# Kernel optimization log

Measured on AMD Instinct MI355X. Metric: run time of the kernel, lower is better.

The kernel has to match this reference:

```python
import jax, jax.numpy as jnp
import numpy as np

NEG_SLOPE = 0.2  # PyG GATConv default negative_slope


def gat_layer(x, W, a_src, a_dst, bias, src, dst, num_nodes):
    # x: [N, Fin], W: [Fin, H*C], a_src/a_dst: [H, C], bias: [C]
    H, C = a_src.shape
    h = (x @ W).reshape(num_nodes, H, C)                      # [N, H, C]
    alpha_src = jnp.einsum('nhc,hc->nh', h, a_src)            # [N, H]
    alpha_dst = jnp.einsum('nhc,hc->nh', h, a_dst)            # [N, H]
    e = jax.nn.leaky_relu(alpha_src[src] + alpha_dst[dst], NEG_SLOPE)  # [E, H]
    # segment softmax over incoming edges of each destination node
    m = jax.ops.segment_max(e, dst, num_segments=num_nodes)  # [N, H]
    p = jnp.exp(e - m[dst])
    denom = jax.ops.segment_sum(p, dst, num_segments=num_nodes)
    alpha = p / denom[dst]                                    # [E, H]
    out = jax.ops.segment_sum(h[src] * alpha[:, :, None], dst,
                              num_segments=num_nodes)         # [N, H, C]
    return out.mean(axis=1) + bias                            # concat=False -> mean


def setup_inputs() -> dict:
    key = jax.random.key(0)
    ks = jax.random.split(key, 8)
    N, E, F, H = 20000, 640000, 128, 4
    s = 0.1  # weight init scale
    return {
        'x': jax.random.normal(ks[0], (N, F), jnp.float32),
        'W1': jax.random.normal(ks[1], (F, H * F), jnp.float32) * s,
        'a_src1': jax.random.normal(ks[2], (H, F), jnp.float32) * s,
        'a_dst1': jax.random.normal(ks[3], (H, F), jnp.float32) * s,
        'b1': jnp.zeros((F,), jnp.float32),
        'W2': jax.random.normal(ks[4], (F, F), jnp.float32) * s,
        'a_src2': jax.random.normal(ks[5], (1, F), jnp.float32) * s,
        'a_dst2': jax.random.normal(ks[6], (1, F), jnp.float32) * s,
        'b2': jnp.zeros((F,), jnp.float32),
        'edge_index': jax.random.randint(ks[7], (2, E), 0, N, jnp.int32),
    }


def reference(x, W1, a_src1, a_dst1, b1, W2, a_src2, a_dst2, b2, edge_index):
    N = x.shape[0]
    loop = jnp.arange(N, dtype=edge_index.dtype)  # add_self_loops=True (PyG default)
    src = jnp.concatenate([edge_index[0], loop])
    dst = jnp.concatenate([edge_index[1], loop])
    h = jax.nn.elu(gat_layer(x, W1, a_src1, a_dst1, b1, src, dst, N))
    out = jax.nn.elu(gat_layer(h, W2, a_src2, a_dst2, b2, src, dst, N))
    return out
```

## Files before the change

### kernel.cpp

```cpp
#include <hip/hip_runtime.h>
#include <hip/hip_bf16.h>


typedef short v8s __attribute__((ext_vector_type(8)));
typedef float v4f __attribute__((ext_vector_type(4)));
typedef float v2f __attribute__((ext_vector_type(2)));

template <int K> struct IC { static constexpr int value = K; };

constexpr int MAXD = 128;
constexpr int EPB = 4096;
constexpr int BINW = 64;

__device__ __forceinline__ void bf2x(unsigned int u, float& lo, float& hi) {
    union { unsigned int i; float f; } a, b;
    a.i = u << 16;
    b.i = u & 0xffff0000u;
    lo = a.f;
    hi = b.f;
}
__device__ __forceinline__ v2f bf2p(unsigned int u) {
    union { unsigned int i; float f; } a, b;
    a.i = u << 16;
    b.i = u & 0xffff0000u;
    return (v2f){a.f, b.f};
}
__device__ __forceinline__ unsigned short f2bf(float f) {
    union { float f; unsigned int i; } v;
    v.f = f;
    unsigned int lsb = (v.i >> 16) & 1u;
    v.i += 0x7fffu + lsb;
    return (unsigned short)(v.i >> 16);
}
__device__ __forceinline__ unsigned int pack2(float a, float b) {
    return (unsigned int)f2bf(a) | ((unsigned int)f2bf(b) << 16);
}

__device__ __forceinline__ void scan512_incl(unsigned int* a, int tid) {
#pragma unroll
    for (int off = 1; off < 512; off <<= 1) {
        unsigned int v0 = (tid >= off) ? a[tid - off] : 0u;
        unsigned int v1 = a[tid + 256 - off];
        __syncthreads();
        a[tid] += v0;
        a[tid + 256] += v1;
        __syncthreads();
    }
}

__launch_bounds__(256)
__global__ void prep_part_kernel(const int* __restrict__ src, const int* __restrict__ dst,
                                 int E, unsigned int* __restrict__ binBuf,
                                 unsigned short* __restrict__ boff,
                                 int Bh,
                                 const float* __restrict__ x,
                                 const float* __restrict__ W1, const float* __restrict__ W2,
                                 const float* __restrict__ as1v, const float* __restrict__ ad1v,
                                 const float* __restrict__ as2v, const float* __restrict__ ad2v,
                                 unsigned short* __restrict__ xb,
                                 unsigned short* __restrict__ Bt1,
                                 unsigned short* __restrict__ Bt2,
                                 float* __restrict__ wsrc1, float* __restrict__ wdst1,
                                 float* __restrict__ wsrc2, float* __restrict__ wdst2,
                                 float* __restrict__ as2, float* __restrict__ ad2, int N) {
    int b = blockIdx.x;
    if (b < Bh) {
        __shared__ unsigned int bh[512];
        __shared__ unsigned int stg[EPB];
        const int tid = threadIdx.x;
        bh[tid] = 0u;
        bh[tid + 256] = 0u;
        __syncthreads();
        const int e0 = b * EPB;
        const int ne = min(EPB, E - e0);

        unsigned int pk[16], ps[16];
#pragma unroll
        for (int k = 0; k < 4; ++k) {
            int rel = (k * 256 + tid) * 4;
            if (rel < ne) {
                int4 s4 = *(const int4*)&src[e0 + rel];
                int4 d4 = *(const int4*)&dst[e0 + rel];
                int ss[4] = {s4.x, s4.y, s4.z, s4.w};
                int dd[4] = {d4.x, d4.y, d4.z, d4.w};
#pragma unroll
                for (int j = 0; j < 4; ++j) {
                    unsigned int bin = (unsigned int)dd[j] >> 6;
                    pk[k * 4 + j] = (unsigned int)ss[j] |
                                    (((unsigned int)dd[j] & 63u) << 15) | (bin << 21);
                    ps[k * 4 + j] = atomicAdd(&bh[bin], 1u);
                }
            } else {
#pragma unroll
                for (int j = 0; j < 4; ++j) pk[k * 4 + j] = 0xffffffffu;
            }
        }
        __syncthreads();
        scan512_incl(bh, tid);
#pragma unroll
        for (int k = 0; k < 16; ++k) {
            unsigned int p = pk[k];
            if (p != 0xffffffffu) {
                unsigned int bin = p >> 21;
                unsigned int lo = bin ? bh[bin - 1] : 0u;
                stg[lo + ps[k]] = p;
            }
        }
        __syncthreads();
        unsigned int* out = binBuf + (size_t)b * EPB;
        for (int j = tid; j < ne; j += 256) out[j] = stg[j];
        unsigned short* bo = boff + (size_t)b * 512;
        bo[tid] = (unsigned short)bh[tid];
        bo[tid + 256] = (unsigned short)bh[tid + 256];
        return;
    }
    b -= Bh;
    const int Bcast = (N * 32 + 255) / 256;
    if (b < Bcast) {
        int i = (b * 256 + threadIdx.x) * 4;
        if (i + 3 < N * 128) {
            float4 v = *(const float4*)&x[i];
            ushort4 o;
            o.x = f2bf(v.x);
            o.y = f2bf(v.y);
            o.z = f2bf(v.z);
            o.w = f2bf(v.w);
            *(ushort4*)&xb[i] = o;
        } else {
            for (; i < N * 128; ++i) xb[i] = f2bf(x[i]);
        }
        return;
    }
    b -= Bcast;
    if (b < 256) {
        int i = b * 256 + threadIdx.x;
        int c = i >> 9;
        int r = i & 511;
        int h = r >> 7, k = r & 127;
        Bt1[i] = f2bf(W1[(size_t)k * 512 + (h << 7) + c] * 0.25f);
        return;
    }
    b -= 256;
    if (b < 64) {
        int i = b * 256 + threadIdx.x;
        int c = i >> 7, k = i & 127;
        Bt2[i] = f2bf(W2[(size_t)k * 128 + c]);
        return;
    }
    b -= 64;
    if (b < 2) {
        int i = b * 256 + threadIdx.x;
        int h = i >> 7, k = i & 127;
        const float* wr = W1 + (size_t)k * 512 + (h << 7);
        const float* as_ = as1v + (h << 7);
        const float* ad_ = ad1v + (h << 7);
        float s1 = 0.f, s2 = 0.f;
        for (int c = 0; c < 128; ++c) {
            float wv = wr[c];
            s1 += wv * as_[c];
            s2 += wv * ad_[c];
        }
        wsrc1[i] = s1;
        wdst1[i] = s2;
        return;
    }
    b -= 2;
    if (b < 1) {
        int k = threadIdx.x;
        if (k < 128) {
            const float* wr = W2 + (size_t)k * 128;
            float s1 = 0.f, s2 = 0.f;
            for (int c = 0; c < 128; ++c) {
                float wv = wr[c];
                s1 += wv * as2v[c];
                s2 += wv * ad2v[c];
            }
            wsrc2[k] = s1;
            wdst2[k] = s2;
        }
        return;
    }
    b -= 1;
    {
        int i = b * 256 + threadIdx.x;
        if (i < N) {
            as2[i] = 0.f;
            ad2[i] = 0.f;
        }
    }
}

__launch_bounds__(256)
__global__ void build_alpha_kernel(const unsigned int* __restrict__ binBuf,
                                   const unsigned short* __restrict__ boff,
                                   unsigned short* __restrict__ slot,
                                   int* __restrict__ cnt, int N, int Bh, int NB,
                                   const unsigned int* __restrict__ xrow,
                                   const float* __restrict__ wsrc,
                                   const float* __restrict__ wdst,
                                   float* __restrict__ asrc, float* __restrict__ adst) {
    if ((int)blockIdx.x < NB) {
        __shared__ unsigned int scnt[BINW];
        __shared__ unsigned short sslot[BINW][MAXD];
        const int tid = threadIdx.x;
        const int b = blockIdx.x;
        if (tid < BINW) {
            scnt[tid] = 1u;
            sslot[tid][0] = (unsigned short)(b * BINW + tid);
        }
        __syncthreads();
        for (int k = tid; k < Bh; k += 256) {
            const unsigned short* bo = boff + (size_t)k * 512;
            unsigned int lo = b ? (unsigned int)bo[b - 1] : 0u;
            unsigned int hi = (unsigned int)bo[b];
            const unsigned int* buf = binBuf + (size_t)k * EPB;
            for (unsigned int j = lo; j < hi; ++j) {
                unsigned int p = buf[j];
                int dl = (int)((p >> 15) & 63u);
                unsigned int pos = atomicAdd(&scnt[dl], 1u);
                if (pos < (unsigned int)MAXD) sslot[dl][pos] = (unsigned short)(p & 0x7fffu);
            }
        }
        __syncthreads();
        const int rows = min(BINW, N - b * BINW);
        const int nq = rows * (MAXD / 8);
        uint4* gdst = (uint4*)(slot + (size_t)b * BINW * MAXD);
        const uint4* lsrc = (const uint4*)&sslot[0][0];
        for (int j = tid; j < nq; j += 256) gdst[j] = lsrc[j];
        if (tid < rows) cnt[b * BINW + tid] = (int)min(scnt[tid], (unsigned int)MAXD);
        return;
    }
    constexpr int H = 4;
    __shared__ float s_wv[2 * H * 128];
    for (int i = threadIdx.x; i < 2 * H * 128; i += 256)
        s_wv[i] = (i < H * 128) ? wsrc[i] : wdst[i - H * 128];
    __syncthreads();
    const int wid = threadIdx.x >> 6, lane = threadIdx.x & 63;
    const int n = (blockIdx.x - NB) * 4 + wid;
    if (n >= N) return;
    unsigned int u = xrow[(size_t)n * 64 + lane];
    float f0, f1;
    bf2x(u, f0, f1);
    float s1[H], s2[H];
#pragma unroll
    for (int h = 0; h < H; ++h) {
        float2 ws = *(const float2*)&s_wv[h * 128 + 2 * lane];
        float2 wd = *(const float2*)&s_wv[H * 128 + h * 128 + 2 * lane];
        s1[h] = f0 * ws.x + f1 * ws.y;
        s2[h] = f0 * wd.x + f1 * wd.y;
    }
#pragma unroll
    for (int off = 32; off; off >>= 1)
#pragma unroll
        for (int h = 0; h < H; ++h) {
            s1[h] += __shfl_xor(s1[h], off);
            s2[h] += __shfl_xor(s2[h], off);
        }
    if (lane == 0) {
#pragma unroll
        for (int h = 0; h < H; ++h) {
            asrc[(size_t)n * H + h] = s1[h];
            adst[(size_t)n * H + h] = s2[h];
        }
    }
}

template <int H, int NPB>
__launch_bounds__(64 * NPB, 4)
__global__ void gat_gather_kernel(const uint4* __restrict__ xrow4,
                                  const float* __restrict__ asrc,
                                  const float* __restrict__ adst,
                                  const int* __restrict__ cnt,
                                  const unsigned short* __restrict__ slot,
                                  uint4* __restrict__ Sb4,
                                  int N) {
    static_assert(H == 4 || H == 1, "H");
    const int wid = threadIdx.x >> 6, lane = threadIdx.x & 63;
    const int q = lane >> 4, l16 = lane & 15;
    const int n = blockIdx.x * NPB + wid;
    if (n >= N) return;

    __shared__ int s_src_all[NPB][64];
    __shared__ float s_w_all[NPB][64 * H];
    int* s_src = s_src_all[wid];
    float* s_w = s_w_all[wid];

    const int base = n * MAXD;
    const int deg = min(cnt[n], MAXD);

    float adst_n[H];
#pragma unroll
    for (int h = 0; h < H; ++h) adst_n[h] = adst[(size_t)n * H + h];

    float sum_h[H] = {};
    v2f acc[4 * H];
#pragma unroll
    for (int i = 0; i < 4 * H; ++i) acc[i] = (v2f){0.f, 0.f};

    auto do_batch = [&](int j0, auto kc) {
        constexpr int KK = decltype(kc)::value;
        int ss[KK];
        uint4 d[KK];
#pragma unroll
        for (int k = 0; k < KK; ++k) ss[k] = s_src[j0 + k * 4 + q];
#pragma unroll
        for (int k = 0; k < KK; ++k) d[k] = xrow4[(size_t)ss[k] * 16 + l16];
#pragma unroll
        for (int k = 0; k < KK; ++k) {
            v2f f2[4];
            f2[0] = bf2p(d[k].x);
            f2[1] = bf2p(d[k].y);
            f2[2] = bf2p(d[k].z);
            f2[3] = bf2p(d[k].w);
            if constexpr (H == 4) {
                float4 w = *(const float4*)&s_w[(j0 + k * 4 + q) * 4];
                v2f w0 = (v2f){w.x, w.x}, w1 = (v2f){w.y, w.y};
                v2f w2 = (v2f){w.z, w.z}, w3 = (v2f){w.w, w.w};
#pragma unroll
                for (int j = 0; j < 4; ++j) {
                    acc[j] += w0 * f2[j];
                    acc[4 + j] += w1 * f2[j];
                    acc[8 + j] += w2 * f2[j];
                    acc[12 + j] += w3 * f2[j];
                }
            } else {
                float w = s_w[j0 + k * 4 + q];
                v2f w0 = (v2f){w, w};
#pragma unroll
                for (int j = 0; j < 4; ++j) acc[j] += w0 * f2[j];
            }
        }
    };

    for (int i0 = 0; i0 < deg; i0 += 64) {
        const int cntc = min(64, deg - i0);
        {
            const bool valid = lane < cntc;
            int idx = i0 + (valid ? lane : (cntc - 1));
            int s = (int)slot[base + idx];
            s_src[lane] = s;
            if constexpr (H == 4) {
                float4 av = ((const float4*)asrc)[s];
                float ev[4] = {av.x, av.y, av.z, av.w};
#pragma unroll
                for (int hh = 0; hh < 4; ++hh) {
                    float e = ev[hh] + adst_n[hh];
                    e = e > 0.f ? e : 0.2f * e;
                    float wv = valid ? __expf(e) : 0.f;
                    s_w[lane * 4 + hh] = wv;
                    sum_h[hh] += wv;
                }
            } else {
                float e = asrc[s] + adst_n[0];
                e = e > 0.f ? e : 0.2f * e;
                float wv = valid ? __expf(e) : 0.f;
                s_w[lane] = wv;
                sum_h[0] += wv;
            }
        }
        __threadfence_block();

        int j0 = 0;
        for (; j0 + 32 <= cntc; j0 += 32) do_batch(j0, IC<8>{});
        const int rem = cntc - j0;
        if (rem > 0) {
            switch ((rem + 3) >> 2) {
                case 1: do_batch(j0, IC<1>{}); break;
                case 2: do_batch(j0, IC<2>{}); break;
                case 3: do_batch(j0, IC<3>{}); break;
                case 4: do_batch(j0, IC<4>{}); break;
                case 5: do_batch(j0, IC<5>{}); break;
                case 6: do_batch(j0, IC<6>{}); break;
                case 7: do_batch(j0, IC<7>{}); break;
                default: do_batch(j0, IC<8>{}); break;
            }
        }
    }

#pragma unroll
    for (int i = 0; i < 4 * H; ++i) {
        acc[i][0] += __shfl_xor(acc[i][0], 16);
        acc[i][1] += __shfl_xor(acc[i][1], 16);
        acc[i][0] += __shfl_xor(acc[i][0], 32);
        acc[i][1] += __shfl_xor(acc[i][1], 32);
    }
#pragma unroll
    for (int off = 32; off; off >>= 1)
#pragma unroll
        for (int h = 0; h < H; ++h) sum_h[h] += __shfl_xor(sum_h[h], off);

    if constexpr (H == 4) {
#pragma unroll
        for (int h = 0; h < 4; ++h) {
            if (q == h) {
                float rd = 1.0f / sum_h[h];
                uint4 o;
                o.x = pack2(acc[h * 4 + 0][0] * rd, acc[h * 4 + 0][1] * rd);
                o.y = pack2(acc[h * 4 + 1][0] * rd, acc[h * 4 + 1][1] * rd);
                o.z = pack2(acc[h * 4 + 2][0] * rd, acc[h * 4 + 2][1] * rd);
                o.w = pack2(acc[h * 4 + 3][0] * rd, acc[h * 4 + 3][1] * rd);
                Sb4[(size_t)n * 64 + h * 16 + l16] = o;
            }
        }
    } else {
        if (q == 0) {
            float rd = 1.0f / sum_h[0];
            uint4 o;
            o.x = pack2(acc[0][0] * rd, acc[0][1] * rd);
            o.y = pack2(acc[1][0] * rd, acc[1][1] * rd);
            o.z = pack2(acc[2][0] * rd, acc[2][1] * rd);
            o.w = pack2(acc[3][0] * rd, acc[3][1] * rd);
            Sb4[(size_t)n * 16 + l16] = o;
        }
    }
}

__device__ __forceinline__ void store_out(float* p, float v) { *p = v; }
__device__ __forceinline__ void store_out(unsigned short* p, float v) { *p = f2bf(v); }

template <typename OT, bool ELU, bool FUSE_A2>
__launch_bounds__(256)
__global__ void gemm_bias_act_kernel(const unsigned short* __restrict__ A,
                                     const unsigned short* __restrict__ Bt,
                                     const float* __restrict__ bias,
                                     OT* __restrict__ C,
                                     const float* __restrict__ ws2,
                                     const float* __restrict__ wd2,
                                     float* __restrict__ as2, float* __restrict__ ad2,
                                     int M, int Nout, int K) {
    constexpr int BK = 32;
    __shared__ unsigned short As[64][40];
    __shared__ unsigned short Bs[64][40];

    const int tid = threadIdx.x;
    const int w = tid >> 6;
    const int lane = tid & 63;
    const int m16 = lane & 15;
    const int kg = lane >> 4;
    const int m0 = blockIdx.y * 64;
    const int n0 = blockIdx.x * 64;

    v4f acc[4];
#pragma unroll
    for (int i = 0; i < 4; ++i) acc[i] = (v4f){0.f, 0.f, 0.f, 0.f};

    const int srow = tid >> 2;
    const int sseg = tid & 3;
    const int arow_g = min(m0 + srow, M - 1);
    const unsigned short* Ap = &A[(size_t)arow_g * K + sseg * 8];
    const unsigned short* Bp = &Bt[(size_t)(n0 + srow) * K + sseg * 8];

    for (int k0 = 0; k0 < K; k0 += BK) {
        uint4 av = *(const uint4*)(Ap + k0);
        uint4 bv = *(const uint4*)(Bp + k0);
        __syncthreads();
        *(uint4*)&As[srow][sseg * 8] = av;
        *(uint4*)&Bs[srow][sseg * 8] = bv;
        __syncthreads();
        v8s a = *(const v8s*)&As[w * 16 + m16][kg * 8];
#pragma unroll
        for (int i = 0; i < 4; ++i) {
            v8s b = *(const v8s*)&Bs[i * 16 + m16][kg * 8];
            acc[i] = __builtin_amdgcn_mfma_f32_16x16x32_bf16(a, b, acc[i], 0, 0, 0);
        }
    }

    float pr_s[4] = {}, pr_d[4] = {};
#pragma unroll
    for (int i = 0; i < 4; ++i) {
        const int col = n0 + i * 16 + m16;
        const float bv = bias[col];
        float w2s = 0.f, w2d = 0.f;
        if constexpr (FUSE_A2) {
            w2s = ws2[col];
            w2d = wd2[col];
        }
#pragma unroll
        for (int r = 0; r < 4; ++r) {
            int row = m0 + w * 16 + kg * 4 + r;
            if (row < M) {
                float val = acc[i][r] + bv;
                if constexpr (ELU) val = val > 0.f ? val : (__expf(val) - 1.0f);
                store_out(&C[(size_t)row * Nout + col], val);
                if constexpr (FUSE_A2) {
                    pr_s[r] += val * w2s;
                    pr_d[r] += val * w2d;
                }
            }
        }
    }
    if constexpr (FUSE_A2) {
#pragma unroll
        for (int off = 1; off < 16; off <<= 1)
#pragma unroll
            for (int r = 0; r < 4; ++r) {
                pr_s[r] += __shfl_xor(pr_s[r], off);
                pr_d[r] += __shfl_xor(pr_d[r], off);
            }
        if (m16 == 0) {
#pragma unroll
            for (int r = 0; r < 4; ++r) {
                int row = m0 + w * 16 + kg * 4 + r;
                if (row < M) {
                    atomicAdd(&as2[row], pr_s[r]);
                    atomicAdd(&ad2[row], pr_d[r]);
                }
            }
        }
    }
}


extern "C" void kernel_launch(void* const* d_in, const int* in_sizes, int n_in,
                              void* d_out, int out_size, void* d_ws, size_t ws_size,
                              hipStream_t stream) {
    const float* x = (const float*)d_in[0];
    const float* W1 = (const float*)d_in[1];
    const float* a_src1 = (const float*)d_in[2];
    const float* a_dst1 = (const float*)d_in[3];
    const float* b1 = (const float*)d_in[4];
    const float* W2 = (const float*)d_in[5];
    const float* a_src2 = (const float*)d_in[6];
    const float* a_dst2 = (const float*)d_in[7];
    const float* b2 = (const float*)d_in[8];
    const int* edge = (const int*)d_in[9];
    float* out = (float*)d_out;

    constexpr int F = 128, H = 4;
    const int N = in_sizes[0] / F;
    const int E = in_sizes[9] / 2;
    const int Bh = (E + EPB - 1) / EPB;
    const int NB = (N + BINW - 1) / BINW;

    char* ws = (char*)d_ws;
    size_t o = 0;
    auto take = [&](size_t bytes) {
        char* p = ws + o;
        o = (o + bytes + 255) & ~(size_t)255;
        return p;
    };
    int* cnt = (int*)take((size_t)N * 4);
    unsigned short* slot = (unsigned short*)take((size_t)N * MAXD * 2);
    unsigned int* binBuf = (unsigned int*)take((size_t)Bh * EPB * 4);
    unsigned short* boff = (unsigned short*)take((size_t)Bh * 512 * 2);
    unsigned short* xb = (unsigned short*)take((size_t)N * F * 2);
    unsigned short* Bt1 = (unsigned short*)take((size_t)F * H * F * 2);
    unsigned short* Bt2 = (unsigned short*)take((size_t)F * F * 2);
    float* wsrc1 = (float*)take((size_t)H * F * 4);
    float* wdst1 = (float*)take((size_t)H * F * 4);
    float* wsrc2 = (float*)take((size_t)F * 4);
    float* wdst2 = (float*)take((size_t)F * 4);
    float* as1 = (float*)take((size_t)N * H * 4);
    float* ad1 = (float*)take((size_t)N * H * 4);
    unsigned short* Sb1 = (unsigned short*)take((size_t)N * H * F * 2);
    unsigned short* h2b = (unsigned short*)take((size_t)N * F * 2);
    float* as2 = (float*)take((size_t)N * 4);
    float* ad2 = (float*)take((size_t)N * 4);
    unsigned short* S2b = (unsigned short*)take((size_t)N * F * 2);
    (void)ws_size;

    const int* esrc = edge;
    const int* edst = edge + E;

    const int Bcast = (N * 32 + 255) / 256;
    const int Bzero = (N + 255) / 256;
    hipLaunchKernelGGL(prep_part_kernel, dim3(Bh + Bcast + 256 + 64 + 2 + 1 + Bzero), dim3(256),
                       0, stream, esrc, edst, E, binBuf, boff, Bh, x, W1, W2, a_src1, a_dst1,
                       a_src2, a_dst2, xb, Bt1, Bt2, wsrc1, wdst1, wsrc2, wdst2, as2, ad2, N);

    const int Balpha = (N + 3) / 4;
    hipLaunchKernelGGL(build_alpha_kernel, dim3(NB + Balpha), dim3(256), 0, stream, binBuf,
                       boff, slot, cnt, N, Bh, NB, (const unsigned int*)xb, wsrc1, wdst1, as1,
                       ad1);

    hipLaunchKernelGGL((gat_gather_kernel<H, 4>), dim3((N + 3) / 4), dim3(256), 0, stream,
                       (const uint4*)xb, as1, ad1, cnt, slot, (uint4*)Sb1, N);
    hipLaunchKernelGGL((gemm_bias_act_kernel<unsigned short, true, true>),
                       dim3(F / 64, (N + 63) / 64), dim3(256), 0, stream, Sb1, Bt1, b1, h2b,
                       wsrc2, wdst2, as2, ad2, N, F, H * F);

    hipLaunchKernelGGL((gat_gather_kernel<1, 4>), dim3((N + 3) / 4), dim3(256), 0, stream,
                       (const uint4*)h2b, as2, ad2, cnt, slot, (uint4*)S2b, N);
    hipLaunchKernelGGL((gemm_bias_act_kernel<float, true, false>), dim3(F / 64, (N + 63) / 64),
                       dim3(256), 0, stream, S2b, Bt2, b2, out, nullptr, nullptr, nullptr,
                       nullptr, N, F, F);
}
```

Before: 180.0 us.

## Fuse layer-2 output GEMM, bias and ELU into the H=1 gather kernel

```diff
diff --git a/kernel.cpp b/kernel.cpp
--- a/kernel.cpp
+++ b/kernel.cpp
@@ -273,17 +273,29 @@
                                   const int* __restrict__ cnt,
                                   const unsigned short* __restrict__ slot,
                                   uint4* __restrict__ Sb4,
+                                  const unsigned short* __restrict__ W2b,
+                                  const float* __restrict__ bias2,
+                                  float* __restrict__ outF,
                                   int N) {
     static_assert(H == 4 || H == 1, "H");
     const int wid = threadIdx.x >> 6, lane = threadIdx.x & 63;
     const int q = lane >> 4, l16 = lane & 15;
     const int n = blockIdx.x * NPB + wid;
-    if (n >= N) return;
 
     __shared__ int s_src_all[NPB][64];
     __shared__ float s_w_all[NPB][64 * H];
+    __shared__ unsigned short sW2[H == 1 ? 128 * 128 : 1];
+    __shared__ float s_out_all[NPB][H == 1 ? 128 : 1];
     int* s_src = s_src_all[wid];
     float* s_w = s_w_all[wid];
+
+    if constexpr (H == 1) {
+        const uint4* g = (const uint4*)W2b;
+        uint4* l = (uint4*)sW2;
+        for (int i = threadIdx.x; i < 128 * 128 / 8; i += 256) l[i] = g[i];
+        __syncthreads();
+    }
+    if (n >= N) return;
 
     const int base = n * MAXD;
     const int deg = min(cnt[n], MAXD);
@@ -403,15 +415,47 @@
             }
         }
     } else {
+        float* s_out = s_out_all[wid];
+        const float rd = 1.0f / sum_h[0];
         if (q == 0) {
-            float rd = 1.0f / sum_h[0];
-            uint4 o;
-            o.x = pack2(acc[0][0] * rd, acc[0][1] * rd);
-            o.y = pack2(acc[1][0] * rd, acc[1][1] * rd);
-            o.z = pack2(acc[2][0] * rd, acc[2][1] * rd);
-            o.w = pack2(acc[3][0] * rd, acc[3][1] * rd);
-            Sb4[(size_t)n * 16 + l16] = o;
-        }
+#pragma unroll
+            for (int j = 0; j < 4; ++j) {
+                s_out[l16 * 8 + 2 * j] = acc[j][0] * rd;
+                s_out[l16 * 8 + 2 * j + 1] = acc[j][1] * rd;
+            }
+        }
+        __threadfence_block();
+        const int c0 = lane << 1;
+        const uint4* wrow0 = (const uint4*)&sW2[(size_t)c0 * 128];
+        const uint4* wrow1 = (const uint4*)&sW2[(size_t)(c0 + 1) * 128];
+        const float4* sv4 = (const float4*)s_out;
+        v2f o = (v2f){0.f, 0.f};
+#pragma unroll
+        for (int ii = 0; ii < 16; ++ii) {
+            const int idx = (ii + lane) & 15;
+            uint4 w0v = wrow0[idx];
+            uint4 w1v = wrow1[idx];
+            float4 sa = sv4[idx * 2];
+            float4 sb = sv4[idx * 2 + 1];
+            v2f a0 = bf2p(w0v.x), a1 = bf2p(w0v.y), a2 = bf2p(w0v.z), a3 = bf2p(w0v.w);
+            v2f b0 = bf2p(w1v.x), b1 = bf2p(w1v.y), b2 = bf2p(w1v.z), b3 = bf2p(w1v.w);
+            o += (v2f){a0[0], b0[0]} * (v2f){sa.x, sa.x};
+            o += (v2f){a0[1], b0[1]} * (v2f){sa.y, sa.y};
+            o += (v2f){a1[0], b1[0]} * (v2f){sa.z, sa.z};
+            o += (v2f){a1[1], b1[1]} * (v2f){sa.w, sa.w};
+            o += (v2f){a2[0], b2[0]} * (v2f){sb.x, sb.x};
+            o += (v2f){a2[1], b2[1]} * (v2f){sb.y, sb.y};
+            o += (v2f){a3[0], b3[0]} * (v2f){sb.z, sb.z};
+            o += (v2f){a3[1], b3[1]} * (v2f){sb.w, sb.w};
+        }
+        float o0 = o[0] + bias2[c0];
+        float o1 = o[1] + bias2[c0 + 1];
+        o0 = o0 > 0.f ? o0 : (__expf(o0) - 1.0f);
+        o1 = o1 > 0.f ? o1 : (__expf(o1) - 1.0f);
+        float2 ov;
+        ov.x = o0;
+        ov.y = o1;
+        *(float2*)&outF[(size_t)n * 128 + c0] = ov;
     }
 }
 
@@ -556,7 +600,6 @@
     unsigned short* h2b = (unsigned short*)take((size_t)N * F * 2);
     float* as2 = (float*)take((size_t)N * 4);
     float* ad2 = (float*)take((size_t)N * 4);
-    unsigned short* S2b = (unsigned short*)take((size_t)N * F * 2);
     (void)ws_size;
 
     const int* esrc = edge;
@@ -574,14 +617,12 @@
                        ad1);
 
     hipLaunchKernelGGL((gat_gather_kernel<H, 4>), dim3((N + 3) / 4), dim3(256), 0, stream,
-                       (const uint4*)xb, as1, ad1, cnt, slot, (uint4*)Sb1, N);
+                       (const uint4*)xb, as1, ad1, cnt, slot, (uint4*)Sb1, nullptr, nullptr,
+                       nullptr, N);
     hipLaunchKernelGGL((gemm_bias_act_kernel<unsigned short, true, true>),
                        dim3(F / 64, (N + 63) / 64), dim3(256), 0, stream, Sb1, Bt1, b1, h2b,
                        wsrc2, wdst2, as2, ad2, N, F, H * F);
 
     hipLaunchKernelGGL((gat_gather_kernel<1, 4>), dim3((N + 3) / 4), dim3(256), 0, stream,
-                       (const uint4*)h2b, as2, ad2, cnt, slot, (uint4*)S2b, N);
-    hipLaunchKernelGGL((gemm_bias_act_kernel<float, true, false>), dim3(F / 64, (N + 63) / 64),
-                       dim3(256), 0, stream, S2b, Bt2, b2, out, nullptr, nullptr, nullptr,
-                       nullptr, N, F, F);
-}
+                       (const uint4*)h2b, as2, ad2, cnt, slot, nullptr, Bt2, b2, out, N);
+}
```

New measurement: 189.0 us. 5.0% more time.

## Merge six GAT kernel launches into one cooperative persistent kernel with grid syncs

Applied to the files above, without the earlier changes.

```diff
diff --git a/kernel.cpp b/kernel.cpp
--- a/kernel.cpp
+++ b/kernel.cpp
@@ -1,5 +1,8 @@
 #include <hip/hip_runtime.h>
 #include <hip/hip_bf16.h>
+#include <hip/hip_cooperative_groups.h>
+
+namespace cg = cooperative_groups;
 
 
 typedef short v8s __attribute__((ext_vector_type(8)));
@@ -11,6 +14,7 @@
 constexpr int MAXD = 128;
 constexpr int EPB = 4096;
 constexpr int BINW = 64;
+constexpr int SMEM_BYTES = 18688;
 
 __device__ __forceinline__ void bf2x(unsigned int u, float& lo, float& hi) {
     union { unsigned int i; float f; } a, b;
@@ -48,195 +52,220 @@
     }
 }
 
-__launch_bounds__(256)
-__global__ void prep_part_kernel(const int* __restrict__ src, const int* __restrict__ dst,
-                                 int E, unsigned int* __restrict__ binBuf,
-                                 unsigned short* __restrict__ boff,
-                                 int Bh,
-                                 const float* __restrict__ x,
-                                 const float* __restrict__ W1, const float* __restrict__ W2,
-                                 const float* __restrict__ as1v, const float* __restrict__ ad1v,
-                                 const float* __restrict__ as2v, const float* __restrict__ ad2v,
-                                 unsigned short* __restrict__ xb,
-                                 unsigned short* __restrict__ Bt1,
-                                 unsigned short* __restrict__ Bt2,
-                                 float* __restrict__ wsrc1, float* __restrict__ wdst1,
-                                 float* __restrict__ wsrc2, float* __restrict__ wdst2,
-                                 float* __restrict__ as2, float* __restrict__ ad2, int N) {
-    int b = blockIdx.x;
-    if (b < Bh) {
-        __shared__ unsigned int bh[512];
-        __shared__ unsigned int stg[EPB];
-        const int tid = threadIdx.x;
-        bh[tid] = 0u;
-        bh[tid + 256] = 0u;
-        __syncthreads();
-        const int e0 = b * EPB;
-        const int ne = min(EPB, E - e0);
-
-        unsigned int pk[16], ps[16];
-#pragma unroll
-        for (int k = 0; k < 4; ++k) {
-            int rel = (k * 256 + tid) * 4;
-            if (rel < ne) {
-                int4 s4 = *(const int4*)&src[e0 + rel];
-                int4 d4 = *(const int4*)&dst[e0 + rel];
-                int ss[4] = {s4.x, s4.y, s4.z, s4.w};
-                int dd[4] = {d4.x, d4.y, d4.z, d4.w};
-#pragma unroll
-                for (int j = 0; j < 4; ++j) {
-                    unsigned int bin = (unsigned int)dd[j] >> 6;
-                    pk[k * 4 + j] = (unsigned int)ss[j] |
-                                    (((unsigned int)dd[j] & 63u) << 15) | (bin << 21);
-                    ps[k * 4 + j] = atomicAdd(&bh[bin], 1u);
-                }
-            } else {
-#pragma unroll
-                for (int j = 0; j < 4; ++j) pk[k * 4 + j] = 0xffffffffu;
-            }
-        }
-        __syncthreads();
-        scan512_incl(bh, tid);
-#pragma unroll
-        for (int k = 0; k < 16; ++k) {
-            unsigned int p = pk[k];
-            if (p != 0xffffffffu) {
-                unsigned int bin = p >> 21;
-                unsigned int lo = bin ? bh[bin - 1] : 0u;
-                stg[lo + ps[k]] = p;
-            }
-        }
-        __syncthreads();
-        unsigned int* out = binBuf + (size_t)b * EPB;
-        for (int j = tid; j < ne; j += 256) out[j] = stg[j];
-        unsigned short* bo = boff + (size_t)b * 512;
-        bo[tid] = (unsigned short)bh[tid];
-        bo[tid + 256] = (unsigned short)bh[tid + 256];
-        return;
-    }
-    b -= Bh;
+struct GatParams {
+    const int* esrc;
+    const int* edst;
+    int E;
+    unsigned int* binBuf;
+    unsigned short* boff;
+    int Bh;
+    const float* x;
+    const float* W1;
+    const float* W2;
+    const float* as1v;
+    const float* ad1v;
+    const float* as2v;
+    const float* ad2v;
+    unsigned short* xb;
+    unsigned short* Bt1;
+    unsigned short* Bt2;
+    float* wsrc1;
+    float* wdst1;
+    float* wsrc2;
+    float* wdst2;
+    float* as1;
+    float* ad1;
+    float* as2;
+    float* ad2;
+    unsigned short* slot;
+    int* cnt;
+    int NB;
+    unsigned short* Sb1;
+    unsigned short* h2b;
+    unsigned short* S2b;
+    float* outp;
+    const float* b1;
+    const float* b2;
+    int N;
+};
+
+
+__device__ __forceinline__ void partition_vb(int b, int tid, unsigned char* smem,
+                                             const int* __restrict__ src,
+                                             const int* __restrict__ dst, int E,
+                                             unsigned int* __restrict__ binBuf,
+                                             unsigned short* __restrict__ boff) {
+    unsigned int* bh = (unsigned int*)smem;
+    unsigned int* stg = (unsigned int*)(smem + 2048);
+    bh[tid] = 0u;
+    bh[tid + 256] = 0u;
+    __syncthreads();
+    const int e0 = b * EPB;
+    const int ne = min(EPB, E - e0);
+
+    unsigned int pk[16], ps[16];
+#pragma unroll
+    for (int k = 0; k < 4; ++k) {
+        int rel = (k * 256 + tid) * 4;
+        if (rel < ne) {
+            int4 s4 = *(const int4*)&src[e0 + rel];
+            int4 d4 = *(const int4*)&dst[e0 + rel];
+            int ss[4] = {s4.x, s4.y, s4.z, s4.w};
+            int dd[4] = {d4.x, d4.y, d4.z, d4.w};
+#pragma unroll
+            for (int j = 0; j < 4; ++j) {
+                unsigned int bin = (unsigned int)dd[j] >> 6;
+                pk[k * 4 + j] = (unsigned int)ss[j] |
+                                (((unsigned int)dd[j] & 63u) << 15) | (bin << 21);
+                ps[k * 4 + j] = atomicAdd(&bh[bin], 1u);
+            }
+        } else {
+#pragma unroll
+            for (int j = 0; j < 4; ++j) pk[k * 4 + j] = 0xffffffffu;
+        }
+    }
+    __syncthreads();
+    scan512_incl(bh, tid);
+#pragma unroll
+    for (int k = 0; k < 16; ++k) {
+        unsigned int p = pk[k];
+        if (p != 0xffffffffu) {
+            unsigned int bin = p >> 21;
+            unsigned int lo = bin ? bh[bin - 1] : 0u;
+            stg[lo + ps[k]] = p;
+        }
+    }
+    __syncthreads();
+    unsigned int* out = binBuf + (size_t)b * EPB;
+    for (int j = tid; j < ne; j += 256) out[j] = stg[j];
+    unsigned short* bo = boff + (size_t)b * 512;
+    bo[tid] = (unsigned short)bh[tid];
+    bo[tid + 256] = (unsigned short)bh[tid + 256];
+}
+
+__device__ __forceinline__ void prep_vb(int b, int tid, const GatParams& p) {
+    const int N = p.N;
     const int Bcast = (N * 32 + 255) / 256;
     if (b < Bcast) {
-        int i = (b * 256 + threadIdx.x) * 4;
+        int i = (b * 256 + tid) * 4;
         if (i + 3 < N * 128) {
-            float4 v = *(const float4*)&x[i];
+            float4 v = *(const float4*)&p.x[i];
             ushort4 o;
             o.x = f2bf(v.x);
             o.y = f2bf(v.y);
             o.z = f2bf(v.z);
             o.w = f2bf(v.w);
-            *(ushort4*)&xb[i] = o;
+            *(ushort4*)&p.xb[i] = o;
         } else {
-            for (; i < N * 128; ++i) xb[i] = f2bf(x[i]);
+            for (; i < N * 128; ++i) p.xb[i] = f2bf(p.x[i]);
         }
         return;
     }
     b -= Bcast;
     if (b < 256) {
-        int i = b * 256 + threadIdx.x;
+        int i = b * 256 + tid;
         int c = i >> 9;
         int r = i & 511;
         int h = r >> 7, k = r & 127;
-        Bt1[i] = f2bf(W1[(size_t)k * 512 + (h << 7) + c] * 0.25f);
+        p.Bt1[i] = f2bf(p.W1[(size_t)k * 512 + (h << 7) + c] * 0.25f);
         return;
     }
     b -= 256;
     if (b < 64) {
-        int i = b * 256 + threadIdx.x;
+        int i = b * 256 + tid;
         int c = i >> 7, k = i & 127;
-        Bt2[i] = f2bf(W2[(size_t)k * 128 + c]);
+        p.Bt2[i] = f2bf(p.W2[(size_t)k * 128 + c]);
         return;
     }
     b -= 64;
     if (b < 2) {
-        int i = b * 256 + threadIdx.x;
+        int i = b * 256 + tid;
         int h = i >> 7, k = i & 127;
-        const float* wr = W1 + (size_t)k * 512 + (h << 7);
-        const float* as_ = as1v + (h << 7);
-        const float* ad_ = ad1v + (h << 7);
+        const float* wr = p.W1 + (size_t)k * 512 + (h << 7);
+        const float* as_ = p.as1v + (h << 7);
+        const float* ad_ = p.ad1v + (h << 7);
         float s1 = 0.f, s2 = 0.f;
         for (int c = 0; c < 128; ++c) {
             float wv = wr[c];
             s1 += wv * as_[c];
             s2 += wv * ad_[c];
         }
-        wsrc1[i] = s1;
-        wdst1[i] = s2;
+        p.wsrc1[i] = s1;
+        p.wdst1[i] = s2;
         return;
     }
     b -= 2;
     if (b < 1) {
-        int k = threadIdx.x;
+        int k = tid;
         if (k < 128) {
-            const float* wr = W2 + (size_t)k * 128;
+            const float* wr = p.W2 + (size_t)k * 128;
             float s1 = 0.f, s2 = 0.f;
             for (int c = 0; c < 128; ++c) {
                 float wv = wr[c];
-                s1 += wv * as2v[c];
-                s2 += wv * ad2v[c];
-            }
-            wsrc2[k] = s1;
-            wdst2[k] = s2;
+                s1 += wv * p.as2v[c];
+                s2 += wv * p.ad2v[c];
+            }
+            p.wsrc2[k] = s1;
+            p.wdst2[k] = s2;
         }
         return;
     }
     b -= 1;
     {
-        int i = b * 256 + threadIdx.x;
+        int i = b * 256 + tid;
         if (i < N) {
-            as2[i] = 0.f;
-            ad2[i] = 0.f;
-        }
-    }
-}
-
-__launch_bounds__(256)
-__global__ void build_alpha_kernel(const unsigned int* __restrict__ binBuf,
-                                   const unsigned short* __restrict__ boff,
-                                   unsigned short* __restrict__ slot,
-                                   int* __restrict__ cnt, int N, int Bh, int NB,
-                                   const unsigned int* __restrict__ xrow,
-                                   const float* __restrict__ wsrc,
-                                   const float* __restrict__ wdst,
-                                   float* __restrict__ asrc, float* __restrict__ adst) {
-    if ((int)blockIdx.x < NB) {
-        __shared__ unsigned int scnt[BINW];
-        __shared__ unsigned short sslot[BINW][MAXD];
-        const int tid = threadIdx.x;
-        const int b = blockIdx.x;
-        if (tid < BINW) {
-            scnt[tid] = 1u;
-            sslot[tid][0] = (unsigned short)(b * BINW + tid);
-        }
-        __syncthreads();
-        for (int k = tid; k < Bh; k += 256) {
-            const unsigned short* bo = boff + (size_t)k * 512;
-            unsigned int lo = b ? (unsigned int)bo[b - 1] : 0u;
-            unsigned int hi = (unsigned int)bo[b];
-            const unsigned int* buf = binBuf + (size_t)k * EPB;
-            for (unsigned int j = lo; j < hi; ++j) {
-                unsigned int p = buf[j];
-                int dl = (int)((p >> 15) & 63u);
-                unsigned int pos = atomicAdd(&scnt[dl], 1u);
-                if (pos < (unsigned int)MAXD) sslot[dl][pos] = (unsigned short)(p & 0x7fffu);
-            }
-        }
-        __syncthreads();
-        const int rows = min(BINW, N - b * BINW);
-        const int nq = rows * (MAXD / 8);
-        uint4* gdst = (uint4*)(slot + (size_t)b * BINW * MAXD);
-        const uint4* lsrc = (const uint4*)&sslot[0][0];
-        for (int j = tid; j < nq; j += 256) gdst[j] = lsrc[j];
-        if (tid < rows) cnt[b * BINW + tid] = (int)min(scnt[tid], (unsigned int)MAXD);
-        return;
-    }
+            p.as2[i] = 0.f;
+            p.ad2[i] = 0.f;
+        }
+    }
+}
+
+__device__ __forceinline__ void build_vb(int b, int tid, unsigned char* smem,
+                                         const unsigned int* __restrict__ binBuf,
+                                         const unsigned short* __restrict__ boff,
+                                         unsigned short* __restrict__ slot,
+                                         int* __restrict__ cnt, int N, int Bh) {
+    unsigned int* scnt = (unsigned int*)smem;
+    unsigned short(*sslot)[MAXD] = (unsigned short(*)[MAXD])(smem + 256);
+    if (tid < BINW) {
+        scnt[tid] = 1u;
+        sslot[tid][0] = (unsigned short)(b * BINW + tid);
+    }
+    __syncthreads();
+    for (int k = tid; k < Bh; k += 256) {
+        const unsigned short* bo = boff + (size_t)k * 512;
+        unsigned int lo = b ? (unsigned int)bo[b - 1] : 0u;
+        unsigned int hi = (unsigned int)bo[b];
+        const unsigned int* buf = binBuf + (size_t)k * EPB;
+        for (unsigned int j = lo; j < hi; ++j) {
+            unsigned int pv = buf[j];
+            int dl = (int)((pv >> 15) & 63u);
+            unsigned int pos = atomicAdd(&scnt[dl], 1u);
+            if (pos < (unsigned int)MAXD) sslot[dl][pos] = (unsigned short)(pv & 0x7fffu);
+        }
+    }
+    __syncthreads();
+    const int rows = min(BINW, N - b * BINW);
+    const int nq = rows * (MAXD / 8);
+    uint4* gdst = (uint4*)(slot + (size_t)b * BINW * MAXD);
+    const uint4* lsrc = (const uint4*)&sslot[0][0];
+    for (int j = tid; j < nq; j += 256) gdst[j] = lsrc[j];
+    if (tid < rows) cnt[b * BINW + tid] = (int)min(scnt[tid], (unsigned int)MAXD);
+}
+
+__device__ __forceinline__ void alpha_vb(int vb, int tid, unsigned char* smem,
+                                         const unsigned int* __restrict__ xrow,
+                                         const float* __restrict__ wsrc,
+                                         const float* __restrict__ wdst,
+                                         float* __restrict__ asrc,
+                                         float* __restrict__ adst, int N) {
     constexpr int H = 4;
-    __shared__ float s_wv[2 * H * 128];
-    for (int i = threadIdx.x; i < 2 * H * 128; i += 256)
+    float* s_wv = (float*)smem;
+    for (int i = tid; i < 2 * H * 128; i += 256)
         s_wv[i] = (i < H * 128) ? wsrc[i] : wdst[i - H * 128];
     __syncthreads();
-    const int wid = threadIdx.x >> 6, lane = threadIdx.x & 63;
-    const int n = (blockIdx.x - NB) * 4 + wid;
+    const int wid = tid >> 6, lane = tid & 63;
+    const int n = vb * 4 + wid;
     if (n >= N) return;
     unsigned int u = xrow[(size_t)n * 64 + lane];
     float f0, f1;
@@ -265,25 +294,22 @@
     }
 }
 
-template <int H, int NPB>
-__launch_bounds__(64 * NPB, 4)
-__global__ void gat_gather_kernel(const uint4* __restrict__ xrow4,
-                                  const float* __restrict__ asrc,
-                                  const float* __restrict__ adst,
-                                  const int* __restrict__ cnt,
-                                  const unsigned short* __restrict__ slot,
-                                  uint4* __restrict__ Sb4,
-                                  int N) {
+template <int H>
+__device__ __forceinline__ void gather_vb(int vb, int tid, unsigned char* smem,
+                                          const uint4* __restrict__ xrow4,
+                                          const float* __restrict__ asrc,
+                                          const float* __restrict__ adst,
+                                          const int* __restrict__ cnt,
+                                          const unsigned short* __restrict__ slot,
+                                          uint4* __restrict__ Sb4, int N) {
     static_assert(H == 4 || H == 1, "H");
-    const int wid = threadIdx.x >> 6, lane = threadIdx.x & 63;
+    constexpr int NPB = 4;
+    const int wid = tid >> 6, lane = tid & 63;
     const int q = lane >> 4, l16 = lane & 15;
-    const int n = blockIdx.x * NPB + wid;
+    const int n = vb * NPB + wid;
+    int* s_src = (int*)smem + wid * 64;
+    float* s_w = (float*)(smem + NPB * 64 * 4) + wid * 64 * H;
     if (n >= N) return;
-
-    __shared__ int s_src_all[NPB][64];
-    __shared__ float s_w_all[NPB][64 * H];
-    int* s_src = s_src_all[wid];
-    float* s_w = s_w_all[wid];
 
     const int base = n * MAXD;
     const int deg = min(cnt[n], MAXD);
@@ -419,26 +445,25 @@
 __device__ __forceinline__ void store_out(unsigned short* p, float v) { *p = f2bf(v); }
 
 template <typename OT, bool ELU, bool FUSE_A2>
-__launch_bounds__(256)
-__global__ void gemm_bias_act_kernel(const unsigned short* __restrict__ A,
-                                     const unsigned short* __restrict__ Bt,
-                                     const float* __restrict__ bias,
-                                     OT* __restrict__ C,
-                                     const float* __restrict__ ws2,
-                                     const float* __restrict__ wd2,
-                                     float* __restrict__ as2, float* __restrict__ ad2,
-                                     int M, int Nout, int K) {
+__device__ __forceinline__ void gemm_vb(int bx, int by, int tid, unsigned char* smem,
+                                        const unsigned short* __restrict__ A,
+                                        const unsigned short* __restrict__ Bt,
+                                        const float* __restrict__ bias,
+                                        OT* __restrict__ C,
+                                        const float* __restrict__ ws2,
+                                        const float* __restrict__ wd2,
+                                        float* __restrict__ as2, float* __restrict__ ad2,
+                                        int M, int Nout, int K) {
     constexpr int BK = 32;
-    __shared__ unsigned short As[64][40];
-    __shared__ unsigned short Bs[64][40];
-
-    const int tid = threadIdx.x;
+    unsigned short(*As)[40] = (unsigned short(*)[40])smem;
+    unsigned short(*Bs)[40] = (unsigned short(*)[40])(smem + 5120);
+
     const int w = tid >> 6;
     const int lane = tid & 63;
     const int m16 = lane & 15;
     const int kg = lane >> 4;
-    const int m0 = blockIdx.y * 64;
-    const int n0 = blockIdx.x * 64;
+    const int m0 = by * 64;
+    const int n0 = bx * 64;
 
     v4f acc[4];
 #pragma unroll
@@ -506,6 +531,82 @@
                     atomicAdd(&ad2[row], pr_d[r]);
                 }
             }
+        }
+    }
+}
+
+__launch_bounds__(256, 4)
+__global__ void gat_mega_kernel(GatParams p) {
+    __shared__ __align__(16) unsigned char smem[SMEM_BYTES];
+    cg::grid_group grid = cg::this_grid();
+    const int tid = threadIdx.x;
+    const int bid = (int)blockIdx.x;
+    const int nblk = (int)gridDim.x;
+    const int N = p.N;
+
+    {
+        const int Bcast = (N * 32 + 255) / 256;
+        const int Bzero = (N + 255) / 256;
+        const int tot = p.Bh + Bcast + 256 + 64 + 2 + 1 + Bzero;
+        for (int vb = bid; vb < tot; vb += nblk) {
+            if (vb < p.Bh) {
+                __syncthreads();
+                partition_vb(vb, tid, smem, p.esrc, p.edst, p.E, p.binBuf, p.boff);
+            } else {
+                prep_vb(vb - p.Bh, tid, p);
+            }
+        }
+    }
+    grid.sync();
+
+    {
+        const int Balpha = (N + 3) / 4;
+        const int tot = p.NB + Balpha;
+        for (int vb = bid; vb < tot; vb += nblk) {
+            __syncthreads();
+            if (vb < p.NB)
+                build_vb(vb, tid, smem, p.binBuf, p.boff, p.slot, p.cnt, N, p.Bh);
+            else
+                alpha_vb(vb - p.NB, tid, smem, (const unsigned int*)p.xb, p.wsrc1,
+                         p.wdst1, p.as1, p.ad1, N);
+        }
+    }
+    grid.sync();
+
+    {
+        const int tot = (N + 3) / 4;
+        for (int vb = bid; vb < tot; vb += nblk)
+            gather_vb<4>(vb, tid, smem, (const uint4*)p.xb, p.as1, p.ad1, p.cnt,
+                         p.slot, (uint4*)p.Sb1, N);
+    }
+    grid.sync();
+
+    {
+        const int tot = 2 * ((N + 63) / 64);
+        for (int vb = bid; vb < tot; vb += nblk) {
+            __syncthreads();
+            gemm_vb<unsigned short, true, true>(vb & 1, vb >> 1, tid, smem, p.Sb1,
+                                                p.Bt1, p.b1, p.h2b, p.wsrc2, p.wdst2,
+                                                p.as2, p.ad2, N, 128, 512);
+        }
+    }
+    grid.sync();
+
+    {
+        const int tot = (N + 3) / 4;
+        for (int vb = bid; vb < tot; vb += nblk)
+            gather_vb<1>(vb, tid, smem, (const uint4*)p.h2b, p.as2, p.ad2, p.cnt,
+                         p.slot, (uint4*)p.S2b, N);
+    }
+    grid.sync();
+
+    {
+        const int tot = 2 * ((N + 63) / 64);
+        for (int vb = bid; vb < tot; vb += nblk) {
+            __syncthreads();
+            gemm_vb<float, true, false>(vb & 1, vb >> 1, tid, smem, p.S2b, p.Bt2,
+                                        p.b2, p.outp, nullptr, nullptr, nullptr,
+                                        nullptr, N, 128, 128);
         }
     }
 }
@@ -559,29 +660,51 @@
     unsigned short* S2b = (unsigned short*)take((size_t)N * F * 2);
     (void)ws_size;
 
-    const int* esrc = edge;
-    const int* edst = edge + E;
-
-    const int Bcast = (N * 32 + 255) / 256;
-    const int Bzero = (N + 255) / 256;
-    hipLaunchKernelGGL(prep_part_kernel, dim3(Bh + Bcast + 256 + 64 + 2 + 1 + Bzero), dim3(256),
-                       0, stream, esrc, edst, E, binBuf, boff, Bh, x, W1, W2, a_src1, a_dst1,
-                       a_src2, a_dst2, xb, Bt1, Bt2, wsrc1, wdst1, wsrc2, wdst2, as2, ad2, N);
-
-    const int Balpha = (N + 3) / 4;
-    hipLaunchKernelGGL(build_alpha_kernel, dim3(NB + Balpha), dim3(256), 0, stream, binBuf,
-                       boff, slot, cnt, N, Bh, NB, (const unsigned int*)xb, wsrc1, wdst1, as1,
-                       ad1);
-
-    hipLaunchKernelGGL((gat_gather_kernel<H, 4>), dim3((N + 3) / 4), dim3(256), 0, stream,
-                       (const uint4*)xb, as1, ad1, cnt, slot, (uint4*)Sb1, N);
-    hipLaunchKernelGGL((gemm_bias_act_kernel<unsigned short, true, true>),
-                       dim3(F / 64, (N + 63) / 64), dim3(256), 0, stream, Sb1, Bt1, b1, h2b,
-                       wsrc2, wdst2, as2, ad2, N, F, H * F);
-
-    hipLaunchKernelGGL((gat_gather_kernel<1, 4>), dim3((N + 3) / 4), dim3(256), 0, stream,
-                       (const uint4*)h2b, as2, ad2, cnt, slot, (uint4*)S2b, N);
-    hipLaunchKernelGGL((gemm_bias_act_kernel<float, true, false>), dim3(F / 64, (N + 63) / 64),
-                       dim3(256), 0, stream, S2b, Bt2, b2, out, nullptr, nullptr, nullptr,
-                       nullptr, N, F, F);
-}
+    GatParams p;
+    p.esrc = edge;
+    p.edst = edge + E;
+    p.E = E;
+    p.binBuf = binBuf;
+    p.boff = boff;
+    p.Bh = Bh;
+    p.x = x;
+    p.W1 = W1;
+    p.W2 = W2;
+    p.as1v = a_src1;
+    p.ad1v = a_dst1;
+    p.as2v = a_src2;
+    p.ad2v = a_dst2;
+    p.xb = xb;
+    p.Bt1 = Bt1;
+    p.Bt2 = Bt2;
+    p.wsrc1 = wsrc1;
+    p.wdst1 = wdst1;
+    p.wsrc2 = wsrc2;
+    p.wdst2 = wdst2;
+    p.as1 = as1;
+    p.ad1 = ad1;
+    p.as2 = as2;
+    p.ad2 = ad2;
+    p.slot = slot;
+    p.cnt = cnt;
+    p.NB = NB;
+    p.Sb1 = Sb1;
+    p.h2b = h2b;
+    p.S2b = S2b;
+    p.outp = out;
+    p.b1 = b1;
+    p.b2 = b2;
+    p.N = N;
+
+    int bpc = 0;
+    if (hipOccupancyMaxActiveBlocksPerMultiprocessor(&bpc, gat_mega_kernel, 256, 0) !=
+            hipSuccess ||
+        bpc <= 0)
+        bpc = 2;
+    if (bpc > 8) bpc = 8;
+    const int grid = bpc * 256;
+
+    void* kargs[] = {(void*)&p};
+    hipLaunchCooperativeKernel(reinterpret_cast<void*>(gat_mega_kernel), dim3(grid),
+                               dim3(256), kargs, 0, stream);
+}
```

Measured after the change: 507.7 us. 182% more time.
